# Performance work log

Hardware: AMD Instinct MI355X
Metric: run time of the kernel (lower is better)

## Reference

```python
import jax, jax.numpy as jnp
import numpy as np

E = 1024      # embedding_size
H = 16        # num_head
DQ = DK = DV = 64  # per-head q/k/v size


def setup_inputs() -> dict:
    key = jax.random.key(0)
    ks = jax.random.split(key, 9)
    B, S = 2, 2048
    s = 1.0 / np.sqrt(E)
    return {
        "q": jax.random.normal(ks[0], (B, S, E), jnp.float32),
        "k": jax.random.normal(ks[1], (B, S, E), jnp.float32),
        "v": jax.random.normal(ks[2], (B, S, E), jnp.float32),
        "w_q": jax.random.normal(ks[3], (E, H * DQ), jnp.float32) * s,
        "b_q": jax.random.normal(ks[4], (H * DQ,), jnp.float32) * s,
        "w_k": jax.random.normal(ks[5], (E, H * DK), jnp.float32) * s,
        "b_k": jax.random.normal(ks[6], (H * DK,), jnp.float32) * s,
        "w_v": jax.random.normal(ks[7], (E, H * DV), jnp.float32) * s,
        "b_v": jax.random.normal(ks[8], (H * DV,), jnp.float32) * s,
    }


def reference(q, k, v, w_q, b_q, w_k, b_k, w_v, b_v):
    B, Sq, _ = q.shape
    Sk = k.shape[1]
    # projections -> [B, S, H, d] -> [B, H, S, d]
    qh = (q @ w_q + b_q).reshape(B, Sq, H, DQ).transpose(0, 2, 1, 3)
    kh = (k @ w_k + b_k).reshape(B, Sk, H, DK).transpose(0, 2, 1, 3)
    vh = (v @ w_v + b_v).reshape(B, Sk, H, DV).transpose(0, 2, 1, 3)
    # scaled dot-product attention; scores [B, H, Sq, Sk]
    scores = jnp.einsum("bhqd,bhkd->bhqk", qh, kh) / jnp.sqrt(jnp.float32(DQ))
    weights = jax.nn.softmax(scores, axis=-1)
    out = jnp.einsum("bhqk,bhkd->bhqd", weights, vh)  # [B, H, Sq, DV]
    return out.transpose(0, 2, 1, 3).reshape(B, Sq, H * DV)
```

## Files before the change

kernel.cpp:

```cpp
#include <hip/hip_runtime.h>
#include <hip/hip_bf16.h>

typedef __bf16 bf16_t;
typedef bf16_t bf16x8 __attribute__((ext_vector_type(8)));
typedef bf16_t bf16x4 __attribute__((ext_vector_type(4)));
typedef short  short4v __attribute__((ext_vector_type(4)));
typedef float  f32x4  __attribute__((ext_vector_type(4)));

#define MFMA16(a,b,c) __builtin_amdgcn_mfma_f32_16x16x32_bf16(a, b, c, 0, 0, 0)

static __device__ inline f32x4 mfma_k16(bf16x4 a, bf16x4 b, f32x4 c) {
#if __has_builtin(__builtin_amdgcn_mfma_f32_16x16x16_bf16)
  return __builtin_amdgcn_mfma_f32_16x16x16_bf16(a, b, c, 0, 0, 0);
#else
  return __builtin_amdgcn_mfma_f32_16x16x16bf16_1k(
      __builtin_bit_cast(short4v, a), __builtin_bit_cast(short4v, b), c, 0, 0, 0);
#endif
}

constexpr int S = 2048, H = 16, Dh = 64;
constexpr int N = H * Dh;
constexpr int K = 1024;
constexpr float QSCALE = 0.125f * 1.4426950408889634f;

static __device__ inline void load_lds16(const bf16_t* g, bf16_t* l) {
  __builtin_amdgcn_global_load_lds(
      (const __attribute__((address_space(1))) void*)g,
      (__attribute__((address_space(3))) void*)l, 16, 0, 0);
}

static __device__ inline ushort f2bb(float x) {
  bf16_t h = (bf16_t)x;
  return __builtin_bit_cast(ushort, h);
}

__global__ __launch_bounds__(256) void prep(
    const float* __restrict__ q, const float* __restrict__ k,
    const float* __restrict__ v,
    const float* __restrict__ wq, const float* __restrict__ wk,
    const float* __restrict__ wv,
    bf16_t* __restrict__ xq, bf16_t* __restrict__ xk, bf16_t* __restrict__ xv,
    bf16_t* __restrict__ wtq, bf16_t* __restrict__ wtk, bf16_t* __restrict__ wtv) {
  __shared__ ushort tile[64][68];
  int bx = blockIdx.x, t = threadIdx.x;
  if (bx < 6144) {
    int z = bx >> 11, bb = bx & 2047;
    const float* xi = z == 0 ? q : z == 1 ? k : v;
    bf16_t*      xo = z == 0 ? xq : z == 1 ? xk : xv;
    size_t idx = ((size_t)bb * 256 + t) * 8;
    float4 a = *(const float4*)&xi[idx];
    float4 b = *(const float4*)&xi[idx + 4];
    bf16x8 w;
    w[0] = (bf16_t)a.x; w[1] = (bf16_t)a.y; w[2] = (bf16_t)a.z; w[3] = (bf16_t)a.w;
    w[4] = (bf16_t)b.x; w[5] = (bf16_t)b.y; w[6] = (bf16_t)b.z; w[7] = (bf16_t)b.w;
    *(bf16x8*)&xo[idx] = w;
  } else {
    int zz = bx - 6144;
    int z = zz >> 8, bb = zz & 255;
    const float* wi = z == 0 ? wq : z == 1 ? wk : wv;
    ushort*      wo = (ushort*)(z == 0 ? wtq : z == 1 ? wtk : wtv);
    int k0 = (bb >> 4) * 64, n0 = (bb & 15) * 64;
    for (int i = 0; i < 4; ++i) {
      int idx4 = (i * 256 + t) * 4;
      int r = idx4 >> 6, c = idx4 & 63;
      float4 vv = *(const float4*)&wi[(size_t)(k0 + r) * N + n0 + c];
      tile[r][c] = f2bb(vv.x); tile[r][c + 1] = f2bb(vv.y);
      tile[r][c + 2] = f2bb(vv.z); tile[r][c + 3] = f2bb(vv.w);
    }
    __syncthreads();
    for (int i = 0; i < 4; ++i) {
      int idx4 = (i * 256 + t) * 4;
      int r = idx4 >> 6, c = idx4 & 63;
      ushort4 vv;
      vv.x = tile[c][r]; vv.y = tile[c + 1][r];
      vv.z = tile[c + 2][r]; vv.w = tile[c + 3][r];
      *(ushort4*)&wo[(size_t)(n0 + r) * K + k0 + c] = vv;
    }
  }
}

__global__ __launch_bounds__(256) void proj_gemm(
    const bf16_t* __restrict__ xq, const bf16_t* __restrict__ xk,
    const bf16_t* __restrict__ xv,
    const bf16_t* __restrict__ wtq, const bf16_t* __restrict__ wtk,
    const bf16_t* __restrict__ wtv,
    const float* __restrict__ bq, const float* __restrict__ bk,
    const float* __restrict__ bv,
    bf16_t* __restrict__ qh, bf16_t* __restrict__ kh, bf16_t* __restrict__ vt) {
  int mode = blockIdx.z;
  const bf16_t* X  = mode == 0 ? xq  : mode == 1 ? xk  : wtv;
  const bf16_t* Wt = mode == 0 ? wtq : mode == 1 ? wtk : xv;
  const float*  Bi = mode == 0 ? bq  : mode == 1 ? bk  : bv;

  __shared__ bf16_t Ash[128][64];
  __shared__ bf16_t Bsh[128][64];

  int tid = threadIdx.x;
  int wave = tid >> 6, lane = tid & 63;
  int lr = lane & 15, lg = lane >> 4;
  int lrow = lane >> 3, lcol = (lane & 7) * 8;
  int m0 = (mode < 2 ? blockIdx.y : blockIdx.x) * 128;
  int n0 = (mode < 2 ? blockIdx.x : blockIdx.y) * 128;
  int wm = (wave >> 1) * 64, wn = (wave & 1) * 64;

  f32x4 acc[4][4];
  for (int i = 0; i < 4; ++i)
    for (int j = 0; j < 4; ++j) acc[i][j] = (f32x4){0.f, 0.f, 0.f, 0.f};

  for (int ko = 0; ko < K / 64; ++ko) {
    __syncthreads();
    for (int j = 0; j < 4; ++j) {
      int r = wave * 32 + j * 8 + lrow;
      load_lds16(&X [(size_t)(m0 + r) * K + ko * 64 + lcol], &Ash[r][lcol]);
      load_lds16(&Wt[(size_t)(n0 + r) * K + ko * 64 + lcol], &Bsh[r][lcol]);
    }
    __syncthreads();
    for (int kk = 0; kk < 2; ++kk) {
      bf16x8 af[4], bfr[4];
      for (int i = 0; i < 4; ++i)
        af[i] = *(const bf16x8*)&Ash[wm + i * 16 + lr][kk * 32 + lg * 8];
      for (int j = 0; j < 4; ++j)
        bfr[j] = *(const bf16x8*)&Bsh[wn + j * 16 + lr][kk * 32 + lg * 8];
      for (int i = 0; i < 4; ++i)
        for (int j = 0; j < 4; ++j)
          acc[i][j] = MFMA16(af[i], bfr[j], acc[i][j]);
    }
  }

  if (mode < 2) {
    float bvv[4];
    for (int j = 0; j < 4; ++j) bvv[j] = Bi[n0 + wn + j * 16 + lr];
    bf16_t* o = (mode == 0) ? qh : kh;
    for (int i = 0; i < 4; ++i)
      for (int j = 0; j < 4; ++j) {
        int n_g = n0 + wn + j * 16 + lr;
        int h = n_g >> 6, d = n_g & 63;
        for (int r = 0; r < 4; ++r) {
          int m_g = m0 + wm + i * 16 + lg * 4 + r;
          int b = m_g >> 11, s = m_g & 2047;
          float v = acc[i][j][r] + bvv[j];
          if (mode == 0) v *= QSCALE;
          o[(((size_t)(b * 16 + h) * 2048) + s) * 64 + d] = (bf16_t)v;
        }
      }
  } else {
    float bm[4][4];
    for (int i = 0; i < 4; ++i)
      for (int r = 0; r < 4; ++r) bm[i][r] = Bi[m0 + wm + i * 16 + lg * 4 + r];
    for (int i = 0; i < 4; ++i)
      for (int j = 0; j < 4; ++j) {
        int n_g = n0 + wn + j * 16 + lr;
        int b = n_g >> 11, s = n_g & 2047;
        for (int r = 0; r < 4; ++r) {
          int w = m0 + wm + i * 16 + lg * 4 + r;
          vt[((size_t)(b * 1024 + w)) * 2048 + s] = (bf16_t)(acc[i][j][r] + bm[i][r]);
        }
      }
  }
}

__global__ __launch_bounds__(256) void attn(
    const bf16_t* __restrict__ qh, const bf16_t* __restrict__ kh,
    const bf16_t* __restrict__ vt, float* __restrict__ out) {
  __shared__ bf16_t kt[64][64];
  __shared__ bf16_t vs[64][64];

  int tid = threadIdx.x, wave = tid >> 6, lane = tid & 63;
  int lr = lane & 15, lg = lane >> 4;
  int lrow = lane >> 3, lchunk = lane & 7;
  int bh = blockIdx.y;
  int q0 = blockIdx.x * 128 + wave * 32;

  const bf16_t* qg = qh + (size_t)bh * S * Dh;
  const bf16_t* kg = kh + (size_t)bh * S * Dh;
  const bf16_t* vg = vt + (size_t)bh * Dh * S;

  bf16x8 bq[2][2];
  for (int ms = 0; ms < 2; ++ms)
    for (int kk = 0; kk < 2; ++kk)
      bq[ms][kk] = *(const bf16x8*)&qg[(size_t)(q0 + ms * 16 + lr) * 64 + kk * 32 + lg * 8];

  bf16x4 ones;
  ones[0] = (bf16_t)1.0f; ones[1] = (bf16_t)1.0f;
  ones[2] = (bf16_t)1.0f; ones[3] = (bf16_t)1.0f;

  f32x4 o_acc[2][4], lacc[2];
  for (int ms = 0; ms < 2; ++ms) {
    lacc[ms] = (f32x4){0.f, 0.f, 0.f, 0.f};
    for (int t = 0; t < 4; ++t) o_acc[ms][t] = (f32x4){0.f, 0.f, 0.f, 0.f};
  }

  for (int it = 0; it < S / 64; ++it) {
    int sk0 = it * 64;
    __syncthreads();
    for (int j = 0; j < 2; ++j) {
      int r = wave * 16 + j * 8 + lrow;
      int gc = (lchunk ^ (r & 7)) * 8;
      load_lds16(&kg[(size_t)(sk0 + r) * 64 + gc], &kt[r][lchunk * 8]);
      load_lds16(&vg[(size_t)r * S + sk0 + gc], &vs[r][lchunk * 8]);
    }
    __syncthreads();

    bf16x8 ak[4][2];
    for (int t = 0; t < 4; ++t)
      for (int kk = 0; kk < 2; ++kk)
        ak[t][kk] = *(const bf16x8*)&kt[t * 16 + lr][((kk * 4 + lg) ^ (lr & 7)) * 8];
    bf16x4 bv[4][4];
    for (int t = 0; t < 4; ++t)
      for (int dt = 0; dt < 4; ++dt)
        bv[t][dt] = *(const bf16x4*)
            &vs[dt * 16 + lr][(((t * 2 + (lg >> 1)) ^ (lr & 7)) * 8) + (lg & 1) * 4];

    for (int ms = 0; ms < 2; ++ms) {
      f32x4 st[4];
      for (int t = 0; t < 4; ++t) st[t] = (f32x4){0.f, 0.f, 0.f, 0.f};
      for (int t = 0; t < 4; ++t)
        for (int kk = 0; kk < 2; ++kk)
          st[t] = MFMA16(ak[t][kk], bq[ms][kk], st[t]);

      bf16x4 pa[4];
      for (int t = 0; t < 4; ++t)
        for (int r = 0; r < 4; ++r)
          pa[t][r] = (bf16_t)exp2f(st[t][r]);

      for (int t = 0; t < 4; ++t) {
        for (int dt = 0; dt < 4; ++dt)
          o_acc[ms][dt] = mfma_k16(pa[t], bv[t][dt], o_acc[ms][dt]);
        lacc[ms] = mfma_k16(pa[t], ones, lacc[ms]);
      }
    }
  }

  int b = bh >> 4, h = bh & 15;
  for (int ms = 0; ms < 2; ++ms)
    for (int r = 0; r < 4; ++r) {
      float inv = 1.f / lacc[ms][r];
      int s_row = q0 + ms * 16 + lg * 4 + r;
      size_t base = ((size_t)(b * S + s_row)) * 1024 + h * 64;
      for (int dt = 0; dt < 4; ++dt)
        out[base + dt * 16 + lr] = o_acc[ms][dt][r] * inv;
    }
}

extern "C" void kernel_launch(void* const* d_in, const int* in_sizes, int n_in,
                              void* d_out, int out_size, void* d_ws, size_t ws_size,
                              hipStream_t stream) {
  const float* q  = (const float*)d_in[0];
  const float* k  = (const float*)d_in[1];
  const float* v  = (const float*)d_in[2];
  const float* wq = (const float*)d_in[3];
  const float* bq = (const float*)d_in[4];
  const float* wk = (const float*)d_in[5];
  const float* bk = (const float*)d_in[6];
  const float* wv = (const float*)d_in[7];
  const float* bv = (const float*)d_in[8];

  bf16_t* ws  = (bf16_t*)d_ws;
  constexpr size_t MW = (size_t)1 << 20;
  constexpr size_t MX = (size_t)4096 * 1024;
  bf16_t* wtq = ws;
  bf16_t* wtk = wtq + MW;
  bf16_t* wtv = wtk + MW;
  bf16_t* xq  = wtv + MW;
  bf16_t* xk  = xq + MX;
  bf16_t* xv  = xk + MX;
  bf16_t* qhd = xv + MX;
  bf16_t* khd = qhd + MX;
  bf16_t* vtd = khd + MX;
  float* out  = (float*)d_out;

  prep<<<6912, 256, 0, stream>>>(q, k, v, wq, wk, wv,
                                 xq, xk, xv, wtq, wtk, wtv);
  proj_gemm<<<dim3(8, 32, 3), 256, 0, stream>>>(xq, xk, xv, wtq, wtk, wtv,
                                                bq, bk, bv, qhd, khd, vtd);
  attn<<<dim3(16, 32), 256, 0, stream>>>(qhd, khd, vtd, out);
}
```

Before: 229.3 us.

## Swizzle projection LDS tiles, stage epilogue through LDS for vector stores, use raw exp2

The projection GEMM now XOR-swizzles its LDS tile columns so the MFMA fragment reads avoid bank conflicts. Its epilogue writes bias-added results into a padded LDS tile first, then emits coalesced 16-byte global stores instead of scattered 2-byte stores. The attention kernel calls the hardware exp2 builtin instead of exp2f, which drops the libm range handling. The costs are extra LDS traffic and two barriers in the epilogue, plus slightly different exp2 behaviour near denormals.

After: 208.4 us. -9.1%, faster.

```diff
diff --git a/kernel.cpp b/kernel.cpp
--- a/kernel.cpp
+++ b/kernel.cpp
@@ -92,13 +92,15 @@
   const bf16_t* Wt = mode == 0 ? wtq : mode == 1 ? wtk : xv;
   const float*  Bi = mode == 0 ? bq  : mode == 1 ? bk  : bv;
 
-  __shared__ bf16_t Ash[128][64];
-  __shared__ bf16_t Bsh[128][64];
+  __shared__ bf16_t smem[17408];
+  bf16_t (*Ash)[64] = (bf16_t(*)[64])smem;
+  bf16_t (*Bsh)[64] = (bf16_t(*)[64])(smem + 8192);
+  bf16_t* Cs = smem;
 
   int tid = threadIdx.x;
   int wave = tid >> 6, lane = tid & 63;
   int lr = lane & 15, lg = lane >> 4;
-  int lrow = lane >> 3, lcol = (lane & 7) * 8;
+  int lrow = lane >> 3, lchunk = lane & 7;
   int m0 = (mode < 2 ? blockIdx.y : blockIdx.x) * 128;
   int n0 = (mode < 2 ? blockIdx.x : blockIdx.y) * 128;
   int wm = (wave >> 1) * 64, wn = (wave & 1) * 64;
@@ -111,51 +113,71 @@
     __syncthreads();
     for (int j = 0; j < 4; ++j) {
       int r = wave * 32 + j * 8 + lrow;
-      load_lds16(&X [(size_t)(m0 + r) * K + ko * 64 + lcol], &Ash[r][lcol]);
-      load_lds16(&Wt[(size_t)(n0 + r) * K + ko * 64 + lcol], &Bsh[r][lcol]);
+      int gc = (lchunk ^ (r & 7)) * 8;
+      load_lds16(&X [(size_t)(m0 + r) * K + ko * 64 + gc], &Ash[r][lchunk * 8]);
+      load_lds16(&Wt[(size_t)(n0 + r) * K + ko * 64 + gc], &Bsh[r][lchunk * 8]);
     }
     __syncthreads();
     for (int kk = 0; kk < 2; ++kk) {
       bf16x8 af[4], bfr[4];
-      for (int i = 0; i < 4; ++i)
-        af[i] = *(const bf16x8*)&Ash[wm + i * 16 + lr][kk * 32 + lg * 8];
-      for (int j = 0; j < 4; ++j)
-        bfr[j] = *(const bf16x8*)&Bsh[wn + j * 16 + lr][kk * 32 + lg * 8];
+      for (int i = 0; i < 4; ++i) {
+        int rr = wm + i * 16 + lr;
+        af[i] = *(const bf16x8*)&Ash[rr][(((kk << 2) | lg) ^ (rr & 7)) * 8];
+      }
+      for (int j = 0; j < 4; ++j) {
+        int rr = wn + j * 16 + lr;
+        bfr[j] = *(const bf16x8*)&Bsh[rr][(((kk << 2) | lg) ^ (rr & 7)) * 8];
+      }
       for (int i = 0; i < 4; ++i)
         for (int j = 0; j < 4; ++j)
           acc[i][j] = MFMA16(af[i], bfr[j], acc[i][j]);
     }
   }
 
+  float badd[4][4][4];
   if (mode < 2) {
     float bvv[4];
     for (int j = 0; j < 4; ++j) bvv[j] = Bi[n0 + wn + j * 16 + lr];
-    bf16_t* o = (mode == 0) ? qh : kh;
     for (int i = 0; i < 4; ++i)
-      for (int j = 0; j < 4; ++j) {
-        int n_g = n0 + wn + j * 16 + lr;
-        int h = n_g >> 6, d = n_g & 63;
-        for (int r = 0; r < 4; ++r) {
-          int m_g = m0 + wm + i * 16 + lg * 4 + r;
-          int b = m_g >> 11, s = m_g & 2047;
-          float v = acc[i][j][r] + bvv[j];
-          if (mode == 0) v *= QSCALE;
-          o[(((size_t)(b * 16 + h) * 2048) + s) * 64 + d] = (bf16_t)v;
-        }
-      }
+      for (int j = 0; j < 4; ++j)
+        for (int r = 0; r < 4; ++r) badd[i][j][r] = bvv[j];
   } else {
-    float bm[4][4];
     for (int i = 0; i < 4; ++i)
-      for (int r = 0; r < 4; ++r) bm[i][r] = Bi[m0 + wm + i * 16 + lg * 4 + r];
-    for (int i = 0; i < 4; ++i)
-      for (int j = 0; j < 4; ++j) {
-        int n_g = n0 + wn + j * 16 + lr;
-        int b = n_g >> 11, s = n_g & 2047;
-        for (int r = 0; r < 4; ++r) {
-          int w = m0 + wm + i * 16 + lg * 4 + r;
-          vt[((size_t)(b * 1024 + w)) * 2048 + s] = (bf16_t)(acc[i][j][r] + bm[i][r]);
-        }
-      }
+      for (int r = 0; r < 4; ++r) {
+        float bm = Bi[m0 + wm + i * 16 + lg * 4 + r];
+        for (int j = 0; j < 4; ++j) badd[i][j][r] = bm;
+      }
+  }
+
+  __syncthreads();
+  for (int i = 0; i < 4; ++i)
+    for (int j = 0; j < 4; ++j)
+      for (int r = 0; r < 4; ++r) {
+        float vvv = acc[i][j][r] + badd[i][j][r];
+        if (mode == 0) vvv *= QSCALE;
+        Cs[(size_t)(wm + i * 16 + lg * 4 + r) * 136 + wn + j * 16 + lr] = (bf16_t)vvv;
+      }
+  __syncthreads();
+
+  bf16_t* o = mode == 0 ? qh : mode == 1 ? kh : vt;
+  for (int p = 0; p < 8; ++p) {
+    int idx = p * 256 + tid;
+    int row = idx >> 4, ch = idx & 15;
+    bf16x8 vv = *(const bf16x8*)&Cs[(size_t)row * 136 + ch * 8];
+    size_t dst;
+    if (mode < 2) {
+      int m_g = m0 + row;
+      int n_g = n0 + ch * 8;
+      int b = m_g >> 11, s = m_g & 2047;
+      int h = n_g >> 6, d = n_g & 63;
+      dst = (((size_t)(b * 16 + h) * 2048) + s) * 64 + d;
+    } else {
+      int w_g = m0 + row;
+      int t_g = n0 + ch * 8;
+      int b = t_g >> 11, s = t_g & 2047;
+      dst = ((size_t)(b * 1024 + w_g)) * 2048 + s;
+    }
+    *(uint4*)&o[dst] = __builtin_bit_cast(uint4, vv);
   }
 }
 
@@ -221,7 +243,7 @@
       bf16x4 pa[4];
       for (int t = 0; t < 4; ++t)
         for (int r = 0; r < 4; ++r)
-          pa[t][r] = (bf16_t)exp2f(st[t][r]);
+          pa[t][r] = (bf16_t)__builtin_amdgcn_exp2f(st[t][r]);
 
       for (int t = 0; t < 4; ++t) {
         for (int dt = 0; dt < 4; ++dt)
```
